# Kernel optimization log

Hardware: AMD Instinct MI355X
Metric: run time of the kernel (lower is better)

## Reference

```python
import jax, jax.numpy as jnp
import numpy as np

N = 50000
E = 800000
HEADS = 4
C = 64  # per-head channels
IN = 256
NEG_SLOPE = 0.2


def setup_inputs() -> dict:
    key = jax.random.key(0)
    k = jax.random.split(key, 6)
    x = jax.random.normal(k[0], (N, IN), dtype=jnp.float32)
    edge_index = jax.random.randint(k[1], (2, E), 0, N, dtype=jnp.int64)
    # Glorot-ish scale for weights
    W = jax.random.normal(k[2], (IN, HEADS * C), dtype=jnp.float32) * (1.0 / np.sqrt(IN))
    att_src = jax.random.normal(k[3], (HEADS, C), dtype=jnp.float32) * (1.0 / np.sqrt(C))
    att_dst = jax.random.normal(k[4], (HEADS, C), dtype=jnp.float32) * (1.0 / np.sqrt(C))
    bias = jax.random.normal(k[5], (HEADS * C,), dtype=jnp.float32) * 0.02
    return {"x": x, "edge_index": edge_index, "W": W, "att_src": att_src,
            "att_dst": att_dst, "bias": bias}


def _gat_forward(x, edge_index, W, att_src, att_dst, bias):
    n = x.shape[0]
    h = (x @ W).reshape(n, HEADS, C)  # [N, H, C]

    # add self loops (PyG default add_self_loops=True)
    loop = jnp.arange(n, dtype=edge_index.dtype)
    src = jnp.concatenate([edge_index[0], loop])  # [E+N]
    dst = jnp.concatenate([edge_index[1], loop])

    # per-node attention contributions  [N, H]
    a_src = jnp.einsum('nhc,hc->nh', h, att_src)
    a_dst = jnp.einsum('nhc,hc->nh', h, att_dst)

    # edge logits with leaky relu  [E+N, H]
    logits = a_src[src] + a_dst[dst]
    logits = jnp.where(logits >= 0, logits, NEG_SLOPE * logits)

    # segment softmax over destination neighborhoods
    seg_max = jax.ops.segment_max(logits, dst, num_segments=n)  # [N, H]
    seg_max = jnp.where(jnp.isfinite(seg_max), seg_max, 0.0)
    ex = jnp.exp(logits - seg_max[dst])
    denom = jax.ops.segment_sum(ex, dst, num_segments=n)  # [N, H]
    alpha = ex / (denom[dst] + 1e-16)  # [E+N, H]

    # weighted scatter-add of source messages
    msgs = alpha[:, :, None] * h[src]  # [E+N, H, C]
    out = jax.ops.segment_sum(msgs, dst, num_segments=n)  # [N, H, C]
    out = out.reshape(n, HEADS * C) + bias
    return jax.nn.relu(out)


def reference(x, edge_index, W, att_src, att_dst, bias):
    return _gat_forward(x, edge_index, W, att_src, att_dst, bias)
```

## Files before the change

### kernel.cpp

```cpp
#include <hip/hip_runtime.h>
#include <hip/hip_bf16.h>
#include <math.h>

#define NEG 0.2f
#define BSH 5
#define EPB 8192

typedef __attribute__((ext_vector_type(4))) float f4;
typedef __attribute__((ext_vector_type(8))) short s8;

__device__ __forceinline__ short f2bf(float f) {
    unsigned u = __float_as_uint(f);
    u += 0x7fff + ((u >> 16) & 1);
    return (short)(u >> 16);
}
__device__ __forceinline__ unsigned pk2(float a, float b) {
    union { __hip_bfloat162 h; unsigned u; } c;
    c.h = __float22bfloat162_rn(make_float2(a, b));
    return c.u;
}
__device__ __forceinline__ float bf2f(unsigned short s) {
    return __uint_as_float(((unsigned)s) << 16);
}

__global__ void prep(const float* __restrict__ W, short* __restrict__ Wt,
                     int* __restrict__ off, int N, int Etot)
{
    int id = blockIdx.x * 256 + threadIdx.x;
    int n = id >> 8, k = id & 255;
    Wt[id] = f2bf(W[k * 256 + n]);
    if (id == 0) off[N] = Etot;
}

__global__ __launch_bounds__(512) void gemm_attn(
    const float* __restrict__ x, const short* __restrict__ Wt,
    const float* __restrict__ att_src, const float* __restrict__ att_dst,
    short* __restrict__ hb, float* __restrict__ a_src_n,
    float* __restrict__ a_dst_n, int M)
{
    __shared__ __align__(16) short xs[128][32];
    const int t = threadIdx.x;
    const int lane = t & 63, wv = t >> 6;
    const int wr = wv >> 2;
    const int hd = wv & 3;
    const int quad = lane >> 4, l15 = lane & 15;
    const int n0 = blockIdx.x * 128;

    const int row = t >> 2, kq = t & 3;
    const bool okr = (n0 + row) < M;
    const float* xp = x + (size_t)(n0 + row) * 256 + kq * 8;

    const short* wbase = Wt + (size_t)(hd * 64 + l15) * 256 + quad * 8;

    f4 acc[4][4];
#pragma unroll
    for (int i = 0; i < 4; ++i)
#pragma unroll
        for (int j = 0; j < 4; ++j) acc[i][j] = (f4)(0.f);

    for (int ks = 0; ks < 8; ++ks) {
        float4 v0 = {}, v1 = {};
        if (okr) { const float4* p = (const float4*)(xp + ks * 32); v0 = p[0]; v1 = p[1]; }
        __syncthreads();
        uint4 u = { pk2(v0.x, v0.y), pk2(v0.z, v0.w), pk2(v1.x, v1.y), pk2(v1.z, v1.w) };
        *(uint4*)&xs[row][kq * 8] = u;
        __syncthreads();

        s8 af[4], bf[4];
#pragma unroll
        for (int i = 0; i < 4; ++i)
            af[i] = *(const s8*)(wbase + (size_t)(i * 16) * 256 + ks * 32);
#pragma unroll
        for (int j = 0; j < 4; ++j)
            bf[j] = *(const s8*)&xs[wr * 64 + j * 16 + l15][quad * 8];
#pragma unroll
        for (int i = 0; i < 4; ++i)
#pragma unroll
            for (int j = 0; j < 4; ++j)
                acc[i][j] = __builtin_amdgcn_mfma_f32_16x16x32_bf16(af[i], bf[j], acc[i][j], 0, 0, 0);
    }

    float asv[4][4], adv[4][4];
#pragma unroll
    for (int i = 0; i < 4; ++i)
#pragma unroll
        for (int rr = 0; rr < 4; ++rr) {
            asv[i][rr] = att_src[hd * 64 + i * 16 + quad * 4 + rr];
            adv[i][rr] = att_dst[hd * 64 + i * 16 + quad * 4 + rr];
        }

#pragma unroll
    for (int j = 0; j < 4; ++j) {
        const int node = n0 + wr * 64 + j * 16 + l15;
        const bool ok = node < M;
        float ps = 0.f, pd = 0.f;
#pragma unroll
        for (int i = 0; i < 4; ++i)
#pragma unroll
            for (int rr = 0; rr < 4; ++rr) {
                float v = acc[i][j][rr];
                ps = fmaf(v, asv[i][rr], ps);
                pd = fmaf(v, adv[i][rr], pd);
            }
        ps += __shfl_xor(ps, 16); ps += __shfl_xor(ps, 32);
        pd += __shfl_xor(pd, 16); pd += __shfl_xor(pd, 32);
        if (ok && quad == 0) {
            a_src_n[node * 4 + hd] = ps;
            a_dst_n[node * 4 + hd] = pd;
        }
        if (ok) {
#pragma unroll
            for (int i = 0; i < 4; ++i) {
                uint2 pk = make_uint2(pk2(acc[i][j][0], acc[i][j][1]),
                                      pk2(acc[i][j][2], acc[i][j][3]));
                *(uint2*)&hb[(size_t)node * 256 + hd * 64 + i * 16 + quad * 4] = pk;
            }
        }
    }
}

__global__ __launch_bounds__(256) void count2d(const int* __restrict__ ei,
                                               int* __restrict__ hist2d,
                                               int E, int N, int NBUCK, int NB)
{
    extern __shared__ int lh[];
    const int t = threadIdx.x, blk = blockIdx.x;
    for (int b = t; b < NBUCK; b += 256) lh[b] = 0;
    __syncthreads();
    const int e0 = blk * EPB, Etot = E + N;
#pragma unroll 4
    for (int i = 0; i < EPB / 256; ++i) {
        int e = e0 + i * 256 + t;
        if (e < Etot) {
            int dte = (e < E) ? ei[E + e] : (e - E);
            atomicAdd(&lh[dte >> BSH], 1);
        }
    }
    __syncthreads();
    for (int b = t; b < NBUCK; b += 256) hist2d[b * NB + blk] = lh[b];
}

__global__ __launch_bounds__(1024) void scan1(const int* __restrict__ src,
                                              int* __restrict__ dst,
                                              int* __restrict__ bsum, int Ntot)
{
    __shared__ int wsum[16], wexc[16];
    const int t = threadIdx.x, lane = t & 63, w = t >> 6;
    const int idx = blockIdx.x * 1024 + t;
    int v = (idx < Ntot) ? src[idx] : 0;
    int val = v;
#pragma unroll
    for (int o = 1; o < 64; o <<= 1) {
        int u = __shfl_up(val, o);
        if (lane >= o) val += u;
    }
    if (lane == 63) wsum[w] = val;
    __syncthreads();
    if (t < 16) {
        int s = wsum[t];
#pragma unroll
        for (int o = 1; o < 16; o <<= 1) {
            int u = __shfl_up(s, o, 16);
            if (t >= o) s += u;
        }
        wexc[t] = s - wsum[t];
        if (t == 15) bsum[blockIdx.x] = s;
    }
    __syncthreads();
    if (idx < Ntot) dst[idx] = wexc[w] + val - v;
}

__global__ __launch_bounds__(1024) void scan2v(const int* __restrict__ bsum,
                                               int* __restrict__ bexc, int nb)
{
    __shared__ int wsum[16], wexc[16];
    const int t = threadIdx.x, lane = t & 63, w = t >> 6;
    int v = (t < nb) ? bsum[t] : 0;
    int val = v;
#pragma unroll
    for (int o = 1; o < 64; o <<= 1) {
        int u = __shfl_up(val, o);
        if (lane >= o) val += u;
    }
    if (lane == 63) wsum[w] = val;
    __syncthreads();
    if (t < 16) {
        int s = wsum[t];
#pragma unroll
        for (int o = 1; o < 16; o <<= 1) {
            int u = __shfl_up(s, o, 16);
            if (t >= o) s += u;
        }
        wexc[t] = s - wsum[t];
    }
    __syncthreads();
    if (t < nb) bexc[t] = wexc[w] + val - v;
}

__global__ __launch_bounds__(256) void scatter2(const int* __restrict__ ei,
                                                const int* __restrict__ scanned,
                                                const int* __restrict__ bexc,
                                                unsigned* __restrict__ bucketed,
                                                int E, int N, int NBUCK, int NB)
{
    extern __shared__ int lcur[];
    const int t = threadIdx.x, blk = blockIdx.x;
    for (int b = t; b < NBUCK; b += 256) {
        int idx = b * NB + blk;
        lcur[b] = scanned[idx] + bexc[idx >> 10];
    }
    __syncthreads();
    const int e0 = blk * EPB, Etot = E + N;
#pragma unroll 4
    for (int i = 0; i < EPB / 256; ++i) {
        int e = e0 + i * 256 + t;
        if (e < Etot) {
            int src, dte;
            if (e < E) { src = ei[e]; dte = ei[E + e]; }
            else       { src = e - E; dte = src; }
            int pos = atomicAdd(&lcur[dte >> BSH], 1);
            bucketed[pos] = (unsigned)src | ((unsigned)(dte & 31) << 20);
        }
    }
}

__global__ __launch_bounds__(256) void csr_build(
    const unsigned* __restrict__ bucketed, const int* __restrict__ scanned,
    const int* __restrict__ bexc, int* __restrict__ off, int* __restrict__ csr,
    int N, int NB, int NBUCK, int Etot)
{
    __shared__ unsigned est[2048];
    __shared__ int ldeg[32], loff[32], lcur[32];
    const int t = threadIdx.x, b = blockIdx.x;

    const int i0 = b * NB;
    const int gbase = scanned[i0] + bexc[i0 >> 10];
    int gend;
    if (b + 1 == NBUCK) gend = Etot;
    else { int i1 = (b + 1) * NB; gend = scanned[i1] + bexc[i1 >> 10]; }
    int cnt = gend - gbase;
    if (cnt > 2048) cnt = 2048;

    if (t < 32) ldeg[t] = 0;
    __syncthreads();
    for (int i = t; i < cnt; i += 256) {
        unsigned en = bucketed[gbase + i];
        est[i] = en;
        atomicAdd(&ldeg[en >> 20], 1);
    }
    __syncthreads();
    if (t < 32) {
        int v = ldeg[t], val = v;
#pragma unroll
        for (int o = 1; o < 32; o <<= 1) {
            int u = __shfl_up(val, o, 32);
            if (t >= o) val += u;
        }
        loff[t] = val - v;
        lcur[t] = val - v;
    }
    __syncthreads();
    for (int i = t; i < cnt; i += 256) {
        unsigned en = est[i];
        int pos = atomicAdd(&lcur[en >> 20], 1);
        csr[gbase + pos] = (int)(en & 0xFFFFF);
    }
    if (t < 32) {
        int n = (b << BSH) + t;
        if (n < N) off[n] = gbase + loff[t];
    }
}

__global__ __launch_bounds__(256) void aggregate(const short* __restrict__ hb,
                                                 const float* __restrict__ a_src_n,
                                                 const float* __restrict__ a_dst_n,
                                                 const int* __restrict__ off,
                                                 const int* __restrict__ csr,
                                                 const float* __restrict__ bias,
                                                 float* __restrict__ out, int N)
{
    __shared__ float lds_w[4][64][4];
    __shared__ int   lds_s[4][64];
    const int wv = threadIdx.x >> 6;
    const int lane = threadIdx.x & 63;
    const int half = lane >> 5, l31 = lane & 31;
    const int n = blockIdx.x * 4 + wv;
    if (n >= N) return;

    const int base = off[n];
    const int d = off[n + 1] - base;
    const float4 ad = *(const float4*)(a_dst_n + 4 * n);
    const int hl = l31 >> 3;

    float acc[8] = {0.f, 0.f, 0.f, 0.f, 0.f, 0.f, 0.f, 0.f};
    float4 sum = make_float4(0.f, 0.f, 0.f, 0.f);
    const uint4* hp = (const uint4*)hb;

    for (int c0 = 0; c0 < d; c0 += 64) {
        int j = c0 + lane;
        int s = 0;
        float4 w4 = make_float4(0.f, 0.f, 0.f, 0.f);
        if (j < d) {
            s = csr[base + j];
            float4 as = *(const float4*)(a_src_n + 4 * s);
            float lx = as.x + ad.x; lx = lx >= 0.f ? lx : NEG * lx;
            float ly = as.y + ad.y; ly = ly >= 0.f ? ly : NEG * ly;
            float lz = as.z + ad.z; lz = lz >= 0.f ? lz : NEG * lz;
            float lw = as.w + ad.w; lw = lw >= 0.f ? lw : NEG * lw;
            w4 = make_float4(__expf(lx), __expf(ly), __expf(lz), __expf(lw));
        }
        sum.x += w4.x; sum.y += w4.y; sum.z += w4.z; sum.w += w4.w;
        *(float4*)&lds_w[wv][lane][0] = w4;
        lds_s[wv][lane] = s;
        __builtin_amdgcn_wave_barrier();

        const int cl = (d - c0) < 64 ? (d - c0) : 64;
        int jj = 0;
        for (; jj + 4 <= cl; jj += 4) {
            int   s0 = lds_s[wv][jj + half];
            int   s1 = lds_s[wv][jj + 2 + half];
            float w0 = lds_w[wv][jj + half][hl];
            float w1 = lds_w[wv][jj + 2 + half][hl];
            uint4 v0 = hp[(size_t)s0 * 32 + l31];
            uint4 v1 = hp[(size_t)s1 * 32 + l31];
            acc[0] = fmaf(w0, bf2f((unsigned short)(v0.x & 0xffff)), acc[0]);
            acc[1] = fmaf(w0, bf2f((unsigned short)(v0.x >> 16)),    acc[1]);
            acc[2] = fmaf(w0, bf2f((unsigned short)(v0.y & 0xffff)), acc[2]);
            acc[3] = fmaf(w0, bf2f((unsigned short)(v0.y >> 16)),    acc[3]);
            acc[4] = fmaf(w0, bf2f((unsigned short)(v0.z & 0xffff)), acc[4]);
            acc[5] = fmaf(w0, bf2f((unsigned short)(v0.z >> 16)),    acc[5]);
            acc[6] = fmaf(w0, bf2f((unsigned short)(v0.w & 0xffff)), acc[6]);
            acc[7] = fmaf(w0, bf2f((unsigned short)(v0.w >> 16)),    acc[7]);
            acc[0] = fmaf(w1, bf2f((unsigned short)(v1.x & 0xffff)), acc[0]);
            acc[1] = fmaf(w1, bf2f((unsigned short)(v1.x >> 16)),    acc[1]);
            acc[2] = fmaf(w1, bf2f((unsigned short)(v1.y & 0xffff)), acc[2]);
            acc[3] = fmaf(w1, bf2f((unsigned short)(v1.y >> 16)),    acc[3]);
            acc[4] = fmaf(w1, bf2f((unsigned short)(v1.z & 0xffff)), acc[4]);
            acc[5] = fmaf(w1, bf2f((unsigned short)(v1.z >> 16)),    acc[5]);
            acc[6] = fmaf(w1, bf2f((unsigned short)(v1.w & 0xffff)), acc[6]);
            acc[7] = fmaf(w1, bf2f((unsigned short)(v1.w >> 16)),    acc[7]);
        }
        for (; jj < cl; jj += 2) {
            int   s0 = lds_s[wv][jj + half];
            float w0 = lds_w[wv][jj + half][hl];
            uint4 v0 = hp[(size_t)s0 * 32 + l31];
            acc[0] = fmaf(w0, bf2f((unsigned short)(v0.x & 0xffff)), acc[0]);
            acc[1] = fmaf(w0, bf2f((unsigned short)(v0.x >> 16)),    acc[1]);
            acc[2] = fmaf(w0, bf2f((unsigned short)(v0.y & 0xffff)), acc[2]);
            acc[3] = fmaf(w0, bf2f((unsigned short)(v0.y >> 16)),    acc[3]);
            acc[4] = fmaf(w0, bf2f((unsigned short)(v0.z & 0xffff)), acc[4]);
            acc[5] = fmaf(w0, bf2f((unsigned short)(v0.z >> 16)),    acc[5]);
            acc[6] = fmaf(w0, bf2f((unsigned short)(v0.w & 0xffff)), acc[6]);
            acc[7] = fmaf(w0, bf2f((unsigned short)(v0.w >> 16)),    acc[7]);
        }
        __builtin_amdgcn_wave_barrier();
    }

#pragma unroll
    for (int k = 0; k < 8; ++k) acc[k] += __shfl_xor(acc[k], 32);

#pragma unroll
    for (int o = 32; o > 0; o >>= 1) {
        sum.x += __shfl_xor(sum.x, o);
        sum.y += __shfl_xor(sum.y, o);
        sum.z += __shfl_xor(sum.z, o);
        sum.w += __shfl_xor(sum.w, o);
    }
    float sh = (hl & 2) ? ((hl & 1) ? sum.w : sum.z) : ((hl & 1) ? sum.y : sum.x);
    float ih = 1.f / (sh + 1e-16f);

    if (half == 0) {
        const float4* bp = (const float4*)bias + l31 * 2;
        float4 b0 = bp[0], b1 = bp[1];
        float4 o0, o1;
        o0.x = fmaxf(fmaf(acc[0], ih, b0.x), 0.f);
        o0.y = fmaxf(fmaf(acc[1], ih, b0.y), 0.f);
        o0.z = fmaxf(fmaf(acc[2], ih, b0.z), 0.f);
        o0.w = fmaxf(fmaf(acc[3], ih, b0.w), 0.f);
        o1.x = fmaxf(fmaf(acc[4], ih, b1.x), 0.f);
        o1.y = fmaxf(fmaf(acc[5], ih, b1.y), 0.f);
        o1.z = fmaxf(fmaf(acc[6], ih, b1.z), 0.f);
        o1.w = fmaxf(fmaf(acc[7], ih, b1.w), 0.f);
        float4* op = (float4*)(out + (size_t)n * 256) + l31 * 2;
        op[0] = o0;
        op[1] = o1;
    }
}

extern "C" void kernel_launch(void* const* d_in, const int* in_sizes, int n_in,
                              void* d_out, int out_size, void* d_ws, size_t ws_size,
                              hipStream_t stream)
{
    const float* x       = (const float*)d_in[0];
    const int*   ei      = (const int*)d_in[1];
    const float* W       = (const float*)d_in[2];
    const float* att_src = (const float*)d_in[3];
    const float* att_dst = (const float*)d_in[4];
    const float* bias    = (const float*)d_in[5];
    float* out = (float*)d_out;

    const int N = in_sizes[0] / 256;
    const int E = in_sizes[1] / 2;
    const int Etot = E + N;
    const int NBUCK = (N + 31) >> BSH;
    const int NB = (Etot + EPB - 1) / EPB;
    const int Ntot = NBUCK * NB;
    const int nb1 = (Ntot + 1023) / 1024;

    char* p = (char*)d_ws;
    short*    hb      = (short*)p;    p += (size_t)N * 256 * sizeof(short);
    short*    Wt      = (short*)p;    p += 256 * 256 * sizeof(short);
    float*    a_src_n = (float*)p;    p += (size_t)N * 4 * sizeof(float);
    float*    a_dst_n = (float*)p;    p += (size_t)N * 4 * sizeof(float);
    int*      hist2d  = (int*)p;      p += (size_t)Ntot * sizeof(int);
    int*      scanned = (int*)p;      p += (size_t)Ntot * sizeof(int);
    int*      bsum    = (int*)p;      p += 1024 * sizeof(int);
    int*      bexc    = (int*)p;      p += 1024 * sizeof(int);
    int*      off     = (int*)p;      p += (size_t)(N + 1) * sizeof(int);
    unsigned* bucketed= (unsigned*)p; p += (size_t)Etot * sizeof(unsigned);
    int*      csr     = (int*)p;      p += (size_t)Etot * sizeof(int);

    prep<<<256, 256, 0, stream>>>(W, Wt, off, N, Etot);
    gemm_attn<<<(N + 127) / 128, 512, 0, stream>>>(
        x, Wt, att_src, att_dst, hb, a_src_n, a_dst_n, N);
    count2d<<<NB, 256, NBUCK * sizeof(int), stream>>>(ei, hist2d, E, N, NBUCK, NB);
    scan1<<<nb1, 1024, 0, stream>>>(hist2d, scanned, bsum, Ntot);
    scan2v<<<1, 1024, 0, stream>>>(bsum, bexc, nb1);
    scatter2<<<NB, 256, NBUCK * sizeof(int), stream>>>(ei, scanned, bexc, bucketed,
                                                       E, N, NBUCK, NB);
    csr_build<<<NBUCK, 256, 0, stream>>>(bucketed, scanned, bexc, off, csr,
                                         N, NB, NBUCK, Etot);
    aggregate<<<(N + 3) / 4, 256, 0, stream>>>(hb, a_src_n, a_dst_n, off, csr,
                                               bias, out, N);
}
```

Before: 255.5 us.

## Fuse prep with edge count, double-buffer GEMM tiles, vectorize edge binning

Merges the weight-transpose prep and the destination histogram into one launch, removing a kernel. The GEMM's x tile now uses double-buffered LDS with the next slice prefetched into registers, so each step needs one barrier instead of two. The count and scatter passes read edge indices as int4 on full blocks, and edges-per-block drops from 8192 to 2048 for more parallel blocks. csr_build uses per-wave degree counters to cut LDS atomic contention. The smaller EPB makes the 2D histogram and its scan about four times larger, which adds scan work.

Measured after the change: 233.2 us. 1.1x faster.

```diff
diff --git a/kernel.cpp b/kernel.cpp
--- a/kernel.cpp
+++ b/kernel.cpp
@@ -4,7 +4,7 @@
 
 #define NEG 0.2f
 #define BSH 5
-#define EPB 8192
+#define EPB 2048
 
 typedef __attribute__((ext_vector_type(4))) float f4;
 typedef __attribute__((ext_vector_type(8))) short s8;
@@ -23,13 +23,45 @@
     return __uint_as_float(((unsigned)s) << 16);
 }
 
-__global__ void prep(const float* __restrict__ W, short* __restrict__ Wt,
-                     int* __restrict__ off, int N, int Etot)
-{
-    int id = blockIdx.x * 256 + threadIdx.x;
-    int n = id >> 8, k = id & 255;
-    Wt[id] = f2bf(W[k * 256 + n]);
-    if (id == 0) off[N] = Etot;
+__global__ __launch_bounds__(256) void prep_count(
+    const float* __restrict__ W, short* __restrict__ Wt, int* __restrict__ off,
+    const int* __restrict__ ei, int* __restrict__ hist2d,
+    int E, int N, int NBUCK, int NB, int Etot)
+{
+    const int blk = blockIdx.x, t = threadIdx.x;
+    if (blk < 256) {
+        int id = blk * 256 + t;
+        int n = id >> 8, k = id & 255;
+        Wt[id] = f2bf(W[k * 256 + n]);
+        if (id == 0) off[N] = Etot;
+        return;
+    }
+    extern __shared__ int lh[];
+    const int cblk = blk - 256;
+    for (int b = t; b < NBUCK; b += 256) lh[b] = 0;
+    __syncthreads();
+    const int e0 = cblk * EPB;
+    if (e0 + EPB <= E) {
+#pragma unroll
+        for (int i = 0; i < EPB / 1024; ++i) {
+            int e = e0 + i * 1024 + t * 4;
+            int4 d = *(const int4*)(ei + E + e);
+            atomicAdd(&lh[d.x >> BSH], 1);
+            atomicAdd(&lh[d.y >> BSH], 1);
+            atomicAdd(&lh[d.z >> BSH], 1);
+            atomicAdd(&lh[d.w >> BSH], 1);
+        }
+    } else {
+        for (int i = 0; i < EPB / 256; ++i) {
+            int e = e0 + i * 256 + t;
+            if (e < Etot) {
+                int dte = (e < E) ? ei[E + e] : (e - E);
+                atomicAdd(&lh[dte >> BSH], 1);
+            }
+        }
+    }
+    __syncthreads();
+    for (int b = t; b < NBUCK; b += 256) hist2d[b * NB + cblk] = lh[b];
 }
 
 __global__ __launch_bounds__(512) void gemm_attn(
@@ -38,7 +70,7 @@
     short* __restrict__ hb, float* __restrict__ a_src_n,
     float* __restrict__ a_dst_n, int M)
 {
-    __shared__ __align__(16) short xs[128][32];
+    __shared__ __align__(16) short xs[2][128][32];
     const int t = threadIdx.x;
     const int lane = t & 63, wv = t >> 6;
     const int wr = wv >> 2;
@@ -58,13 +90,20 @@
 #pragma unroll
         for (int j = 0; j < 4; ++j) acc[i][j] = (f4)(0.f);
 
+    float4 v0 = {}, v1 = {};
+    if (okr) { const float4* p = (const float4*)xp; v0 = p[0]; v1 = p[1]; }
+
+    int buf = 0;
+#pragma unroll
     for (int ks = 0; ks < 8; ++ks) {
-        float4 v0 = {}, v1 = {};
-        if (okr) { const float4* p = (const float4*)(xp + ks * 32); v0 = p[0]; v1 = p[1]; }
+        uint4 u = { pk2(v0.x, v0.y), pk2(v0.z, v0.w), pk2(v1.x, v1.y), pk2(v1.z, v1.w) };
+        *(uint4*)&xs[buf][row][kq * 8] = u;
         __syncthreads();
-        uint4 u = { pk2(v0.x, v0.y), pk2(v0.z, v0.w), pk2(v1.x, v1.y), pk2(v1.z, v1.w) };
-        *(uint4*)&xs[row][kq * 8] = u;
-        __syncthreads();
+
+        if (ks < 7 && okr) {
+            const float4* p = (const float4*)(xp + (ks + 1) * 32);
+            v0 = p[0]; v1 = p[1];
+        }
 
         s8 af[4], bf[4];
 #pragma unroll
@@ -72,12 +111,13 @@
             af[i] = *(const s8*)(wbase + (size_t)(i * 16) * 256 + ks * 32);
 #pragma unroll
         for (int j = 0; j < 4; ++j)
-            bf[j] = *(const s8*)&xs[wr * 64 + j * 16 + l15][quad * 8];
+            bf[j] = *(const s8*)&xs[buf][wr * 64 + j * 16 + l15][quad * 8];
 #pragma unroll
         for (int i = 0; i < 4; ++i)
 #pragma unroll
             for (int j = 0; j < 4; ++j)
                 acc[i][j] = __builtin_amdgcn_mfma_f32_16x16x32_bf16(af[i], bf[j], acc[i][j], 0, 0, 0);
+        buf ^= 1;
     }
 
     float asv[4][4], adv[4][4];
@@ -119,27 +159,6 @@
     }
 }
 
-__global__ __launch_bounds__(256) void count2d(const int* __restrict__ ei,
-                                               int* __restrict__ hist2d,
-                                               int E, int N, int NBUCK, int NB)
-{
-    extern __shared__ int lh[];
-    const int t = threadIdx.x, blk = blockIdx.x;
-    for (int b = t; b < NBUCK; b += 256) lh[b] = 0;
-    __syncthreads();
-    const int e0 = blk * EPB, Etot = E + N;
-#pragma unroll 4
-    for (int i = 0; i < EPB / 256; ++i) {
-        int e = e0 + i * 256 + t;
-        if (e < Etot) {
-            int dte = (e < E) ? ei[E + e] : (e - E);
-            atomicAdd(&lh[dte >> BSH], 1);
-        }
-    }
-    __syncthreads();
-    for (int b = t; b < NBUCK; b += 256) hist2d[b * NB + blk] = lh[b];
-}
-
 __global__ __launch_bounds__(1024) void scan1(const int* __restrict__ src,
                                               int* __restrict__ dst,
                                               int* __restrict__ bsum, int Ntot)
@@ -211,15 +230,31 @@
     }
     __syncthreads();
     const int e0 = blk * EPB, Etot = E + N;
-#pragma unroll 4
-    for (int i = 0; i < EPB / 256; ++i) {
-        int e = e0 + i * 256 + t;
-        if (e < Etot) {
-            int src, dte;
-            if (e < E) { src = ei[e]; dte = ei[E + e]; }
-            else       { src = e - E; dte = src; }
-            int pos = atomicAdd(&lcur[dte >> BSH], 1);
-            bucketed[pos] = (unsigned)src | ((unsigned)(dte & 31) << 20);
+    if (e0 + EPB <= E) {
+#pragma unroll
+        for (int i = 0; i < EPB / 1024; ++i) {
+            int e = e0 + i * 1024 + t * 4;
+            int4 s4 = *(const int4*)(ei + e);
+            int4 d4 = *(const int4*)(ei + E + e);
+            int p0 = atomicAdd(&lcur[d4.x >> BSH], 1);
+            bucketed[p0] = (unsigned)s4.x | ((unsigned)(d4.x & 31) << 20);
+            int p1 = atomicAdd(&lcur[d4.y >> BSH], 1);
+            bucketed[p1] = (unsigned)s4.y | ((unsigned)(d4.y & 31) << 20);
+            int p2 = atomicAdd(&lcur[d4.z >> BSH], 1);
+            bucketed[p2] = (unsigned)s4.z | ((unsigned)(d4.z & 31) << 20);
+            int p3 = atomicAdd(&lcur[d4.w >> BSH], 1);
+            bucketed[p3] = (unsigned)s4.w | ((unsigned)(d4.w & 31) << 20);
+        }
+    } else {
+        for (int i = 0; i < EPB / 256; ++i) {
+            int e = e0 + i * 256 + t;
+            if (e < Etot) {
+                int src, dte;
+                if (e < E) { src = ei[e]; dte = ei[E + e]; }
+                else       { src = e - E; dte = src; }
+                int pos = atomicAdd(&lcur[dte >> BSH], 1);
+                bucketed[pos] = (unsigned)src | ((unsigned)(dte & 31) << 20);
+            }
         }
     }
 }
@@ -230,8 +265,8 @@
     int N, int NB, int NBUCK, int Etot)
 {
     __shared__ unsigned est[2048];
-    __shared__ int ldeg[32], loff[32], lcur[32];
-    const int t = threadIdx.x, b = blockIdx.x;
+    __shared__ int ldeg4[4][32], lcur4[4][32], loff[32];
+    const int t = threadIdx.x, wv = t >> 6, b = blockIdx.x;
 
     const int i0 = b * NB;
     const int gbase = scanned[i0] + bexc[i0 >> 10];
@@ -241,28 +276,34 @@
     int cnt = gend - gbase;
     if (cnt > 2048) cnt = 2048;
 
-    if (t < 32) ldeg[t] = 0;
+    if (t < 128) ldeg4[t >> 5][t & 31] = 0;
     __syncthreads();
     for (int i = t; i < cnt; i += 256) {
         unsigned en = bucketed[gbase + i];
         est[i] = en;
-        atomicAdd(&ldeg[en >> 20], 1);
+        atomicAdd(&ldeg4[wv][en >> 20], 1);
     }
     __syncthreads();
     if (t < 32) {
-        int v = ldeg[t], val = v;
+        int d0 = ldeg4[0][t], d1 = ldeg4[1][t], d2 = ldeg4[2][t], d3 = ldeg4[3][t];
+        int tot = d0 + d1 + d2 + d3;
+        int val = tot;
 #pragma unroll
         for (int o = 1; o < 32; o <<= 1) {
             int u = __shfl_up(val, o, 32);
             if (t >= o) val += u;
         }
-        loff[t] = val - v;
-        lcur[t] = val - v;
+        int excl = val - tot;
+        loff[t] = excl;
+        lcur4[0][t] = excl;
+        lcur4[1][t] = excl + d0;
+        lcur4[2][t] = excl + d0 + d1;
+        lcur4[3][t] = excl + d0 + d1 + d2;
     }
     __syncthreads();
     for (int i = t; i < cnt; i += 256) {
         unsigned en = est[i];
-        int pos = atomicAdd(&lcur[en >> 20], 1);
+        int pos = atomicAdd(&lcur4[wv][en >> 20], 1);
         csr[gbase + pos] = (int)(en & 0xFFFFF);
     }
     if (t < 32) {
@@ -420,10 +461,10 @@
     unsigned* bucketed= (unsigned*)p; p += (size_t)Etot * sizeof(unsigned);
     int*      csr     = (int*)p;      p += (size_t)Etot * sizeof(int);
 
-    prep<<<256, 256, 0, stream>>>(W, Wt, off, N, Etot);
+    prep_count<<<256 + NB, 256, NBUCK * sizeof(int), stream>>>(
+        W, Wt, off, ei, hist2d, E, N, NBUCK, NB, Etot);
     gemm_attn<<<(N + 127) / 128, 512, 0, stream>>>(
         x, Wt, att_src, att_dst, hb, a_src_n, a_dst_n, N);
-    count2d<<<NB, 256, NBUCK * sizeof(int), stream>>>(ei, hist2d, E, N, NBUCK, NB);
     scan1<<<nb1, 1024, 0, stream>>>(hist2d, scanned, bsum, Ntot);
     scan2v<<<1, 1024, 0, stream>>>(bsum, bexc, nb1);
     scatter2<<<NB, 256, NBUCK * sizeof(int), stream>>>(ei, scanned, bexc, bucketed,
```
